# Kernel tuning notes

Measured on AMD Instinct MI355X. Metric: run time of the kernel, lower is better.

The kernel has to match this reference:

```python
import jax, jax.numpy as jnp
import numpy as np
import math

N, E = 50000, 800000
HID, EDIM, H = 128, 32, 8
D = HID // H            # head_dim = 16
FFN = 4 * HID           # ModelConstants.FFN_EXPANSION_FACTOR = 4
EPS = 1e-5


def layer_norm(x, g, b):
    mu = jnp.mean(x, axis=-1, keepdims=True)
    var = jnp.var(x, axis=-1, keepdims=True)
    return (x - mu) * jax.lax.rsqrt(var + EPS) * g + b


def setup_inputs() -> dict:
    key = jax.random.key(0)
    ks = jax.random.split(key, 16)
    s = 1.0 / math.sqrt(HID)
    inp = {
        "x": jax.random.normal(ks[0], (N, HID), jnp.float32),
        "edge_index": jax.random.randint(ks[1], (2, E), 0, N, jnp.int32),
        "edge_attr": jax.random.normal(ks[2], (E, EDIM), jnp.float32),
        # projections stored as (in, out): y = x @ W + b (same math as torch Linear)
        "qW": jax.random.normal(ks[3], (HID, HID), jnp.float32) * s,
        "qb": jnp.zeros((HID,), jnp.float32),
        "kW": jax.random.normal(ks[4], (HID, HID), jnp.float32) * s,
        "kb": jnp.zeros((HID,), jnp.float32),
        "vW": jax.random.normal(ks[5], (HID, HID), jnp.float32) * s,
        "vb": jnp.zeros((HID,), jnp.float32),
        "eW": jax.random.normal(ks[6], (EDIM, H), jnp.float32) / math.sqrt(EDIM),
        "eb": jnp.zeros((H,), jnp.float32),
        "oW": jax.random.normal(ks[7], (HID, HID), jnp.float32) * s,
        "ob": jnp.zeros((HID,), jnp.float32),
        "ln1_g": jnp.ones((HID,), jnp.float32),
        "ln1_b": jnp.zeros((HID,), jnp.float32),
        "f1W": jax.random.normal(ks[8], (HID, FFN), jnp.float32) * s,
        "f1b": jnp.zeros((FFN,), jnp.float32),
        "lnf_g": jnp.ones((FFN,), jnp.float32),
        "lnf_b": jnp.zeros((FFN,), jnp.float32),
        "f2W": jax.random.normal(ks[9], (FFN, HID), jnp.float32) / math.sqrt(FFN),
        "f2b": jnp.zeros((HID,), jnp.float32),
        "ln2_g": jnp.ones((HID,), jnp.float32),
        "ln2_b": jnp.zeros((HID,), jnp.float32),
    }
    return inp


def reference(x, edge_index, edge_attr, qW, qb, kW, kb, vW, vb, eW, eb, oW, ob,
              ln1_g, ln1_b, f1W, f1b, lnf_g, lnf_b, f2W, f2b, ln2_g, ln2_b):
    src, dst = edge_index[0], edge_index[1]
    q = (x @ qW + qb).reshape(N, H, D)
    k = (x @ kW + kb).reshape(N, H, D)
    v = (x @ vW + vb).reshape(N, H, D)
    edge_bias = edge_attr @ eW + eb                     # (E, H)
    # per-edge attention scores
    scores = jnp.sum(q[src] * k[dst], axis=-1) / math.sqrt(D) + edge_bias  # (E, H)
    # scatter softmax over edges grouped by dst
    mx = jax.ops.segment_max(scores, dst, num_segments=N)  # (N, H), -inf for empty
    mx = jnp.where(jnp.isinf(mx), jnp.zeros_like(mx), mx)
    ex = jnp.exp(scores - mx[dst])                      # (E, H)
    den = jax.ops.segment_sum(ex, dst, num_segments=N)
    den = jnp.maximum(den, 1e-8)
    attn = ex / den[dst]                                # (E, H)
    # weighted aggregation
    wv = v[src] * attn[:, :, None]                      # (E, H, D)
    out = jax.ops.segment_sum(wv, dst, num_segments=N)  # (N, H, D)
    out = out.reshape(N, HID) @ oW + ob
    x = layer_norm(x + out, ln1_g, ln1_b)
    h = x @ f1W + f1b
    h = jax.nn.gelu(layer_norm(h, lnf_g, lnf_b), approximate=False)
    h = h @ f2W + f2b
    x = layer_norm(x + h, ln2_g, ln2_b)
    return x
```

## Files before the change

kernel.cpp:

```cpp
#include <hip/hip_runtime.h>
#include <math.h>

#define LN_EPS 1e-5f

typedef __attribute__((ext_vector_type(8))) __bf16 bf16x8;
typedef __attribute__((ext_vector_type(4))) float f32x4;

__device__ inline float bf2f(unsigned short u) {
  union { unsigned int i; float f; } x; x.i = ((unsigned int)u) << 16; return x.f;
}
__device__ inline unsigned short f2bf(float f) {
  union { float f; unsigned int i; } x; x.f = f;
  unsigned int r = (x.i + 0x7FFFu + ((x.i >> 16) & 1u)) >> 16;
  return (unsigned short)r;
}
__device__ inline void gload_lds16(const void* g, void* l) {
  __builtin_amdgcn_global_load_lds((const __attribute__((address_space(1))) void*)g,
                                   (__attribute__((address_space(3))) void*)l, 16, 0, 0);
}

__global__ __launch_bounds__(256)
void to_bf16(const float* __restrict__ in, unsigned short* __restrict__ outp, long n) {
  long i = ((long)blockIdx.x * 256 + threadIdx.x) * 4;
  if (i >= n) return;
  float4 v = *(const float4*)&in[i];
  ushort4 o = { f2bf(v.x), f2bf(v.y), f2bf(v.z), f2bf(v.w) };
  *(ushort4*)&outp[i] = o;
}

struct WDesc { const float* W; unsigned short* Wt; int K, M, ntx; };
__global__ __launch_bounds__(256)
void prep_weights(const float* qW, const float* kW, const float* vW, const float* oW,
                  const float* f1W, const float* f2W,
                  unsigned short* qkvWt, unsigned short* oWt,
                  unsigned short* f1Wt, unsigned short* f2Wt,
                  const float* qb, const float* kb, const float* vb, float* qkvbias) {
  const int t = blockIdx.x;
  if (t == 192) {
    int i = threadIdx.x;
    if (i < 128) { qkvbias[i] = qb[i]; qkvbias[128 + i] = kb[i]; }
    else if (i < 256) qkvbias[256 + (i - 128)] = vb[i - 128];
    return;
  }
  const float* W; unsigned short* Wt; int K, M, lt;
  if (t < 64)       { K = 128; M = 128; lt = t & 15;
    if (t < 16)      { W = qW; Wt = qkvWt; }
    else if (t < 32) { W = kW; Wt = qkvWt + 16384; }
    else if (t < 48) { W = vW; Wt = qkvWt + 32768; }
    else             { W = oW; Wt = oWt; } }
  else if (t < 128) { K = 128; M = 512; lt = t - 64; W = f1W; Wt = f1Wt; }
  else              { K = 512; M = 128; lt = t - 128; W = f2W; Wt = f2Wt; }
  const int ktiles = K >> 5;
  const int k0 = (lt % ktiles) * 32, m0 = (lt / ktiles) * 32;
  __shared__ float tb[32][33];
  const int tx = threadIdx.x & 31, ty = threadIdx.x >> 5;
#pragma unroll
  for (int i = 0; i < 32; i += 8)
    tb[ty + i][tx] = W[(size_t)(k0 + ty + i) * M + m0 + tx];
  __syncthreads();
#pragma unroll
  for (int i = 0; i < 32; i += 8)
    Wt[(size_t)(m0 + ty + i) * K + k0 + tx] = f2bf(tb[tx][ty + i]);
}

template<bool OBF>
__global__ __launch_bounds__(256)
void gemm_mfma(const unsigned short* __restrict__ A, const unsigned short* __restrict__ Wt,
               const float* __restrict__ bias, void* __restrict__ Cout,
               int Nr, int K, int M) {
  __shared__ __align__(16) unsigned short As[128 * 64];
  __shared__ __align__(16) unsigned short Bs[128 * 64];
  const int tid = threadIdx.x;
  const int bm = blockIdx.x * 128, bn = blockIdx.y * 128;
  const int lane = tid & 63;
  const int wr = (tid >> 6) >> 1, wc = (tid >> 6) & 1;
  f32x4 acc[4][4] = {};
  const int nkt = K >> 6;
  for (int kt = 0; kt < nkt; ++kt) {
#pragma unroll
    for (int i = 0; i < 4; ++i) {
      int c = tid + i * 256;
      int row = c >> 3;
      int j = (c & 7) ^ (row & 7);
      int ar = bm + row; ar = ar < Nr ? ar : Nr - 1;
      gload_lds16(A + (size_t)ar * K + kt * 64 + j * 8, As + (size_t)c * 8);
      gload_lds16(Wt + (size_t)(bn + row) * K + kt * 64 + j * 8, Bs + (size_t)c * 8);
    }
    __syncthreads();
#pragma unroll
    for (int ks = 0; ks < 2; ++ks) {
      bf16x8 af[4], bfr[4];
#pragma unroll
      for (int f = 0; f < 4; ++f) {
        int rowa = wr * 64 + f * 16 + (lane & 15);
        int ja = (ks * 4 + (lane >> 4)) ^ (rowa & 7);
        af[f] = *(const bf16x8*)(As + rowa * 64 + ja * 8);
        int rowb = wc * 64 + f * 16 + (lane & 15);
        int jb = (ks * 4 + (lane >> 4)) ^ (rowb & 7);
        bfr[f] = *(const bf16x8*)(Bs + rowb * 64 + jb * 8);
      }
#pragma unroll
      for (int fr = 0; fr < 4; ++fr)
#pragma unroll
        for (int fc = 0; fc < 4; ++fc)
          acc[fr][fc] = __builtin_amdgcn_mfma_f32_16x16x32_bf16(af[fr], bfr[fc], acc[fr][fc], 0, 0, 0);
    }
    __syncthreads();
  }
#pragma unroll
  for (int fr = 0; fr < 4; ++fr) {
#pragma unroll
    for (int j = 0; j < 4; ++j) {
      int row = bm + wr * 64 + fr * 16 + (lane >> 4) * 4 + j;
      if (row < Nr) {
#pragma unroll
        for (int fc = 0; fc < 4; ++fc) {
          int col = bn + wc * 64 + fc * 16 + (lane & 15);
          float v = acc[fr][fc][j] + bias[col];
          if (OBF) ((unsigned short*)Cout)[(size_t)row * M + col] = f2bf(v);
          else     ((float*)Cout)[(size_t)row * M + col] = v;
        }
      }
    }
  }
}

template<bool WF32, bool WBF, bool RESBF>
__global__ __launch_bounds__(256)
void gemm_ln(const unsigned short* __restrict__ A, const unsigned short* __restrict__ Wt,
             const float* __restrict__ bias, const void* __restrict__ res,
             const float* __restrict__ g, const float* __restrict__ b,
             float* __restrict__ y, unsigned short* __restrict__ ybf, int Nr, int K) {
  __shared__ __align__(16) unsigned short As[128 * 64];
  __shared__ __align__(16) unsigned short Bs[128 * 64];
  __shared__ float pls[128][2], plss[128][2];
  const int tid = threadIdx.x;
  const int bm = blockIdx.x * 128;
  const int lane = tid & 63;
  const int wr = (tid >> 6) >> 1, wc = (tid >> 6) & 1;
  f32x4 acc[4][4] = {};
  const int nkt = K >> 6;
  for (int kt = 0; kt < nkt; ++kt) {
#pragma unroll
    for (int i = 0; i < 4; ++i) {
      int c = tid + i * 256;
      int row = c >> 3;
      int j = (c & 7) ^ (row & 7);
      int ar = bm + row; ar = ar < Nr ? ar : Nr - 1;
      gload_lds16(A + (size_t)ar * K + kt * 64 + j * 8, As + (size_t)c * 8);
      gload_lds16(Wt + (size_t)row * K + kt * 64 + j * 8, Bs + (size_t)c * 8);
    }
    __syncthreads();
#pragma unroll
    for (int ks = 0; ks < 2; ++ks) {
      bf16x8 af[4], bfr[4];
#pragma unroll
      for (int f = 0; f < 4; ++f) {
        int rowa = wr * 64 + f * 16 + (lane & 15);
        int ja = (ks * 4 + (lane >> 4)) ^ (rowa & 7);
        af[f] = *(const bf16x8*)(As + rowa * 64 + ja * 8);
        int rowb = wc * 64 + f * 16 + (lane & 15);
        int jb = (ks * 4 + (lane >> 4)) ^ (rowb & 7);
        bfr[f] = *(const bf16x8*)(Bs + rowb * 64 + jb * 8);
      }
#pragma unroll
      for (int fr = 0; fr < 4; ++fr)
#pragma unroll
        for (int fc = 0; fc < 4; ++fc)
          acc[fr][fc] = __builtin_amdgcn_mfma_f32_16x16x32_bf16(af[fr], bfr[fc], acc[fr][fc], 0, 0, 0);
    }
    __syncthreads();
  }
#pragma unroll
  for (int fr = 0; fr < 4; ++fr) {
#pragma unroll
    for (int j = 0; j < 4; ++j) {
      const int rl = wr * 64 + fr * 16 + (lane >> 4) * 4 + j;
      const int row = bm + rl;
      const int rowc = row < Nr ? row : Nr - 1;
      float s = 0.f, ss = 0.f;
#pragma unroll
      for (int fc = 0; fc < 4; ++fc) {
        int col = wc * 64 + fc * 16 + (lane & 15);
        float rv = RESBF ? bf2f(((const unsigned short*)res)[(size_t)rowc * 128 + col])
                         : ((const float*)res)[(size_t)rowc * 128 + col];
        float val = acc[fr][fc][j] + bias[col] + rv;
        acc[fr][fc][j] = val;
        s += val; ss += val * val;
      }
      s += __shfl_xor(s, 1); ss += __shfl_xor(ss, 1);
      s += __shfl_xor(s, 2); ss += __shfl_xor(ss, 2);
      s += __shfl_xor(s, 4); ss += __shfl_xor(ss, 4);
      s += __shfl_xor(s, 8); ss += __shfl_xor(ss, 8);
      if ((lane & 15) == 0) { pls[rl][wc] = s; plss[rl][wc] = ss; }
    }
  }
  __syncthreads();
#pragma unroll
  for (int fr = 0; fr < 4; ++fr) {
#pragma unroll
    for (int j = 0; j < 4; ++j) {
      const int rl = wr * 64 + fr * 16 + (lane >> 4) * 4 + j;
      const int row = bm + rl;
      if (row >= Nr) continue;
      const float S = pls[rl][0] + pls[rl][1];
      const float SS = plss[rl][0] + plss[rl][1];
      const float mu = S * (1.f / 128.f);
      const float inv = rsqrtf(SS * (1.f / 128.f) - mu * mu + LN_EPS);
#pragma unroll
      for (int fc = 0; fc < 4; ++fc) {
        int col = wc * 64 + fc * 16 + (lane & 15);
        float o = (acc[fr][fc][j] - mu) * inv * g[col] + b[col];
        if (WF32) y[(size_t)row * 128 + col] = o;
        if (WBF)  ybf[(size_t)row * 128 + col] = f2bf(o);
      }
    }
  }
}

__global__ __launch_bounds__(256)
void edge_hist(const int* __restrict__ ei, int* __restrict__ deg, int E) {
  int e = blockIdx.x * 256 + threadIdx.x;
  if (e < E) atomicAdd(&deg[ei[E + e]], 1);
}

__global__ __launch_bounds__(256)
void deg_block_sum(const int* __restrict__ deg, int* __restrict__ bsum, int N) {
  const int t = threadIdx.x;
  const int beg = blockIdx.x * 2048 + t * 8;
  int s = 0;
#pragma unroll
  for (int j = 0; j < 8; ++j) { int i = beg + j; if (i < N) s += deg[i]; }
#pragma unroll
  for (int off = 32; off; off >>= 1) s += __shfl_xor(s, off);
  __shared__ int ws[4];
  if ((t & 63) == 0) ws[t >> 6] = s;
  __syncthreads();
  if (t == 0) bsum[blockIdx.x] = ws[0] + ws[1] + ws[2] + ws[3];
}

__global__ __launch_bounds__(64)
void scan_bsum(int* __restrict__ bsum, int* __restrict__ offs_last, int nb) {
  const int t = threadIdx.x;
  int v = (t < nb) ? bsum[t] : 0;
  int inc = v;
#pragma unroll
  for (int off = 1; off < 64; off <<= 1) {
    int x = __shfl_up(inc, off);
    if (t >= off) inc += x;
  }
  if (t < nb) bsum[t] = inc - v;
  if (t == 63) *offs_last = inc;
}

__global__ __launch_bounds__(256)
void deg_scan_write(const int* __restrict__ deg, const int* __restrict__ bsum,
                    int* __restrict__ offs, int* __restrict__ pos, int N) {
  const int t = threadIdx.x;
  const int beg = blockIdx.x * 2048 + t * 8;
  int loc[8]; int T = 0;
#pragma unroll
  for (int j = 0; j < 8; ++j) { int i = beg + j; loc[j] = (i < N) ? deg[i] : 0; T += loc[j]; }
  int inc = T;
#pragma unroll
  for (int off = 1; off < 64; off <<= 1) {
    int x = __shfl_up(inc, off);
    if ((t & 63) >= off) inc += x;
  }
  __shared__ int ws[4];
  if ((t & 63) == 63) ws[t >> 6] = inc;
  __syncthreads();
  const int wid = t >> 6;
  int wbase = 0;
  for (int w = 0; w < wid; ++w) wbase += ws[w];
  int base = bsum[blockIdx.x] + wbase + inc - T;
#pragma unroll
  for (int j = 0; j < 8; ++j) {
    int i = beg + j;
    if (i < N) { offs[i] = base; pos[i] = base; base += loc[j]; }
  }
}

__global__ __launch_bounds__(256)
void edge_scatter_bias(const int* __restrict__ ei, int* __restrict__ pos,
                       const float* __restrict__ ea, const float* __restrict__ eW,
                       const float* __restrict__ eb, int* __restrict__ csr_src,
                       unsigned short* __restrict__ ebp, int E) {
  __shared__ float ews[256];
  __shared__ float ebs[8];
  const int tid = threadIdx.x;
  if (tid < 256) ews[tid] = eW[tid];
  if (tid < 8) ebs[tid] = eb[tid];
  __syncthreads();
  int e = blockIdx.x * 256 + tid;
  if (e >= E) return;
  float bias[8];
#pragma unroll
  for (int h = 0; h < 8; ++h) bias[h] = ebs[h];
#pragma unroll
  for (int i4 = 0; i4 < 8; ++i4) {
    float4 a = *(const float4*)&ea[(size_t)e * 32 + i4 * 4];
    float av[4] = {a.x, a.y, a.z, a.w};
#pragma unroll
    for (int j = 0; j < 4; ++j)
#pragma unroll
      for (int h = 0; h < 8; ++h) bias[h] += av[j] * ews[(i4 * 4 + j) * 8 + h];
  }
  int d = ei[E + e];
  int p = atomicAdd(&pos[d], 1);
  csr_src[p] = ei[e];
  union { unsigned short us[8]; uint4 v; } pk;
#pragma unroll
  for (int h = 0; h < 8; ++h) pk.us[h] = f2bf(bias[h]);
  *(uint4*)&ebp[(size_t)p * 8] = pk.v;
}

__global__ __launch_bounds__(256)
void node_agg(const int* __restrict__ csr_src, const int* __restrict__ offs,
              const unsigned short* __restrict__ qkv, const unsigned short* __restrict__ ebp,
              unsigned short* __restrict__ agg, int N) {
  const int wid = threadIdx.x >> 6, lane = threadIdx.x & 63;
  const int h = lane >> 3;
  const long n = (long)blockIdx.x * 4 + wid;
  if (n >= N) return;
  const int off = offs[n], end = offs[n + 1];
  const ushort2 kv2 = *(const ushort2*)&qkv[(size_t)n * 384 + 128 + lane * 2];
  const float k0 = bf2f(kv2.x), k1 = bf2f(kv2.y);
  float acc0 = 0.f, acc1 = 0.f, den = 0.f;
  int i = off;
  for (; i + 8 <= end; i += 8) {
    size_t bb[8];
#pragma unroll
    for (int u = 0; u < 8; ++u) bb[u] = (size_t)csr_src[i + u] * 384;
    ushort2 qv[8], vv[8];
#pragma unroll
    for (int u = 0; u < 8; ++u) qv[u] = *(const ushort2*)&qkv[bb[u] + lane * 2];
#pragma unroll
    for (int u = 0; u < 8; ++u) vv[u] = *(const ushort2*)&qkv[bb[u] + 256 + lane * 2];
    float ebv[8];
#pragma unroll
    for (int u = 0; u < 8; ++u) ebv[u] = bf2f(ebp[(size_t)(i + u) * 8 + h]);
    float p[8];
#pragma unroll
    for (int u = 0; u < 8; ++u) p[u] = bf2f(qv[u].x) * k0 + bf2f(qv[u].y) * k1;
#pragma unroll
    for (int u = 0; u < 8; ++u) {
      p[u] += __shfl_xor(p[u], 1);
      p[u] += __shfl_xor(p[u], 2);
      p[u] += __shfl_xor(p[u], 4);
    }
#pragma unroll
    for (int u = 0; u < 8; ++u) {
      const float ex = __expf(p[u] * 0.25f + ebv[u]);
      den += ex;
      acc0 += bf2f(vv[u].x) * ex;
      acc1 += bf2f(vv[u].y) * ex;
    }
  }
  for (; i + 4 <= end; i += 4) {
    size_t bb[4];
#pragma unroll
    for (int u = 0; u < 4; ++u) bb[u] = (size_t)csr_src[i + u] * 384;
    ushort2 qv[4], vv[4];
#pragma unroll
    for (int u = 0; u < 4; ++u) qv[u] = *(const ushort2*)&qkv[bb[u] + lane * 2];
#pragma unroll
    for (int u = 0; u < 4; ++u) vv[u] = *(const ushort2*)&qkv[bb[u] + 256 + lane * 2];
    float ebv[4];
#pragma unroll
    for (int u = 0; u < 4; ++u) ebv[u] = bf2f(ebp[(size_t)(i + u) * 8 + h]);
    float p[4];
#pragma unroll
    for (int u = 0; u < 4; ++u) p[u] = bf2f(qv[u].x) * k0 + bf2f(qv[u].y) * k1;
#pragma unroll
    for (int u = 0; u < 4; ++u) {
      p[u] += __shfl_xor(p[u], 1);
      p[u] += __shfl_xor(p[u], 2);
      p[u] += __shfl_xor(p[u], 4);
    }
#pragma unroll
    for (int u = 0; u < 4; ++u) {
      const float ex = __expf(p[u] * 0.25f + ebv[u]);
      den += ex;
      acc0 += bf2f(vv[u].x) * ex;
      acc1 += bf2f(vv[u].y) * ex;
    }
  }
  for (; i < end; ++i) {
    const size_t b0 = (size_t)csr_src[i] * 384;
    const ushort2 qa = *(const ushort2*)&qkv[b0 + lane * 2];
    const ushort2 va = *(const ushort2*)&qkv[b0 + 256 + lane * 2];
    float p = bf2f(qa.x) * k0 + bf2f(qa.y) * k1;
    p += __shfl_xor(p, 1);
    p += __shfl_xor(p, 2);
    p += __shfl_xor(p, 4);
    const float ex = __expf(p * 0.25f + bf2f(ebp[(size_t)i * 8 + h]));
    den += ex;
    acc0 += bf2f(va.x) * ex;
    acc1 += bf2f(va.y) * ex;
  }
  const float r = 1.f / fmaxf(den, 1e-8f);
  ushort2 o; o.x = f2bf(acc0 * r); o.y = f2bf(acc1 * r);
  *(ushort2*)&agg[(size_t)n * 128 + lane * 2] = o;
}

__global__ __launch_bounds__(256)
void ln_gelu512(unsigned short* __restrict__ hbuf, const float* __restrict__ g,
                const float* __restrict__ b, int Nr) {
  __shared__ float rs[4], rss[4];
  const long row = blockIdx.x;
  const int tid = threadIdx.x;
  ushort2 u = *(ushort2*)&hbuf[row * 512 + tid * 2];
  float v0 = bf2f(u.x), v1 = bf2f(u.y);
  float s = v0 + v1, ss = v0 * v0 + v1 * v1;
#pragma unroll
  for (int off = 32; off; off >>= 1) { s += __shfl_xor(s, off); ss += __shfl_xor(ss, off); }
  const int wid = tid >> 6, lane = tid & 63;
  if (lane == 0) { rs[wid] = s; rss[wid] = ss; }
  __syncthreads();
  s = rs[0] + rs[1] + rs[2] + rs[3];
  ss = rss[0] + rss[1] + rss[2] + rss[3];
  const float mu = s * (1.f / 512.f);
  const float inv = rsqrtf(ss * (1.f / 512.f) - mu * mu + LN_EPS);
  float t0 = (v0 - mu) * inv * g[tid * 2] + b[tid * 2];
  float t1 = (v1 - mu) * inv * g[tid * 2 + 1] + b[tid * 2 + 1];
  t0 = 0.5f * t0 * (1.f + erff(t0 * 0.70710678118654752f));
  t1 = 0.5f * t1 * (1.f + erff(t1 * 0.70710678118654752f));
  ushort2 o; o.x = f2bf(t0); o.y = f2bf(t1);
  *(ushort2*)&hbuf[row * 512 + tid * 2] = o;
}

extern "C" void kernel_launch(void* const* d_in, const int* in_sizes, int n_in,
                              void* d_out, int out_size, void* d_ws, size_t ws_size,
                              hipStream_t stream) {
  const float* x   = (const float*)d_in[0];
  const int*   ei  = (const int*)d_in[1];
  const float* ea  = (const float*)d_in[2];
  const float* qW  = (const float*)d_in[3];
  const float* qbi = (const float*)d_in[4];
  const float* kW  = (const float*)d_in[5];
  const float* kbi = (const float*)d_in[6];
  const float* vW  = (const float*)d_in[7];
  const float* vbi = (const float*)d_in[8];
  const float* eW  = (const float*)d_in[9];
  const float* eb  = (const float*)d_in[10];
  const float* oW  = (const float*)d_in[11];
  const float* ob  = (const float*)d_in[12];
  const float* ln1_g = (const float*)d_in[13];
  const float* ln1_b = (const float*)d_in[14];
  const float* f1W = (const float*)d_in[15];
  const float* f1b = (const float*)d_in[16];
  const float* lnf_g = (const float*)d_in[17];
  const float* lnf_b = (const float*)d_in[18];
  const float* f2W = (const float*)d_in[19];
  const float* f2b = (const float*)d_in[20];
  const float* ln2_g = (const float*)d_in[21];
  const float* ln2_b = (const float*)d_in[22];
  float* out = (float*)d_out;

  const int N = in_sizes[0] / 128;
  const int E = in_sizes[1] / 2;
  const size_t NH = (size_t)N * 128;

  float* F = (float*)d_ws;
  unsigned short* xbf   = (unsigned short*)F;
  unsigned short* qkvb  = (unsigned short*)(F + NH / 2);
  unsigned short* ebp   = (unsigned short*)(F + 2 * NH);
  unsigned short* aggb  = (unsigned short*)(F + 2 * NH + NH / 2);
  unsigned short* x1bf  = xbf;
  unsigned short* hbufb = (unsigned short*)(F + NH / 2);
  int* ib      = (int*)(F + 4 * NH);
  int* csr_src = ib;
  int* offs    = ib + E;
  int* pos     = ib + E + N + 1;
  int* bsum    = ib + E + 2 * N + 1;
  unsigned short* wt = (unsigned short*)(ib + E + 2 * N + 128);
  unsigned short* qkvWt = wt;
  unsigned short* oWt   = wt + 49152;
  unsigned short* f1Wt  = wt + 65536;
  unsigned short* f2Wt  = wt + 131072;
  float* qkvbias = (float*)(wt + 196608);

  dim3 blk(256);
  dim3 gqkv((N + 127) / 128, 3);
  dim3 g128((N + 127) / 128, 1);
  dim3 gf1((N + 127) / 128, 4);
  const int nb = (N + 2047) / 2048;
  const int ge = (E + 255) / 256;

  to_bf16<<<dim3((int)((NH / 4 + 255) / 256)), blk, 0, stream>>>(x, xbf, (long)NH);
  prep_weights<<<dim3(193), blk, 0, stream>>>(qW, kW, vW, oW, f1W, f2W,
                                              qkvWt, oWt, f1Wt, f2Wt,
                                              qbi, kbi, vbi, qkvbias);

  gemm_mfma<true><<<gqkv, blk, 0, stream>>>(xbf, qkvWt, qkvbias, qkvb, N, 128, 384);

  hipMemsetAsync(pos, 0, (size_t)N * sizeof(int), stream);
  edge_hist<<<dim3(ge), blk, 0, stream>>>(ei, pos, E);
  deg_block_sum<<<dim3(nb), blk, 0, stream>>>(pos, bsum, N);
  scan_bsum<<<dim3(1), dim3(64), 0, stream>>>(bsum, offs + N, nb);
  deg_scan_write<<<dim3(nb), blk, 0, stream>>>(pos, bsum, offs, pos, N);
  edge_scatter_bias<<<dim3(ge), blk, 0, stream>>>(ei, pos, ea, eW, eb, csr_src, ebp, E);

  node_agg<<<dim3((N + 3) / 4), blk, 0, stream>>>(csr_src, offs, qkvb, ebp, aggb, N);

  gemm_ln<false, true, false><<<g128, blk, 0, stream>>>(aggb, oWt, ob, x,
                                                        ln1_g, ln1_b, nullptr, x1bf, N, 128);

  gemm_mfma<true><<<gf1, blk, 0, stream>>>(x1bf, f1Wt, f1b, hbufb, N, 128, 512);
  ln_gelu512<<<dim3(N), blk, 0, stream>>>(hbufb, lnf_g, lnf_b, N);
  gemm_ln<true, false, true><<<g128, blk, 0, stream>>>(hbufb, f2Wt, f2b, x1bf,
                                                       ln2_g, ln2_b, out, nullptr, N, 512);
}
```

Before: 315.6 us.

## Fuse FFN1 GEMM with LayerNorm+GELU and split edge bias from scatter

Replaces the separate FFN1 GEMM and per-row LN+GELU kernel with a single kernel. Each block computes all 512 output columns for 128 rows, accumulates the row statistics, and then rereads its own rows to apply LayerNorm and GELU. Edge-bias computation moves into the histogram pass, writing a sequential bias buffer, so the scatter kernel only permutes 16-byte records. The LN1 GEMM now reads the bf16 copy of x as its residual instead of fp32. The costs are lower grid parallelism in the fused FFN kernel, an extra E×8 bf16 intermediate buffer, and a residual rounded to bf16.

```diff
diff --git a/kernel.cpp b/kernel.cpp
--- a/kernel.cpp
+++ b/kernel.cpp
@@ -28,7 +28,6 @@
   *(ushort4*)&outp[i] = o;
 }
 
-struct WDesc { const float* W; unsigned short* Wt; int K, M, ntx; };
 __global__ __launch_bounds__(256)
 void prep_weights(const float* qW, const float* kW, const float* vW, const float* oW,
                   const float* f1W, const float* f2W,
@@ -219,73 +218,105 @@
 }
 
 __global__ __launch_bounds__(256)
-void edge_hist(const int* __restrict__ ei, int* __restrict__ deg, int E) {
-  int e = blockIdx.x * 256 + threadIdx.x;
-  if (e < E) atomicAdd(&deg[ei[E + e]], 1);
-}
-
-__global__ __launch_bounds__(256)
-void deg_block_sum(const int* __restrict__ deg, int* __restrict__ bsum, int N) {
-  const int t = threadIdx.x;
-  const int beg = blockIdx.x * 2048 + t * 8;
-  int s = 0;
-#pragma unroll
-  for (int j = 0; j < 8; ++j) { int i = beg + j; if (i < N) s += deg[i]; }
-#pragma unroll
-  for (int off = 32; off; off >>= 1) s += __shfl_xor(s, off);
-  __shared__ int ws[4];
-  if ((t & 63) == 0) ws[t >> 6] = s;
-  __syncthreads();
-  if (t == 0) bsum[blockIdx.x] = ws[0] + ws[1] + ws[2] + ws[3];
-}
-
-__global__ __launch_bounds__(64)
-void scan_bsum(int* __restrict__ bsum, int* __restrict__ offs_last, int nb) {
-  const int t = threadIdx.x;
-  int v = (t < nb) ? bsum[t] : 0;
-  int inc = v;
-#pragma unroll
-  for (int off = 1; off < 64; off <<= 1) {
-    int x = __shfl_up(inc, off);
-    if (t >= off) inc += x;
-  }
-  if (t < nb) bsum[t] = inc - v;
-  if (t == 63) *offs_last = inc;
-}
-
-__global__ __launch_bounds__(256)
-void deg_scan_write(const int* __restrict__ deg, const int* __restrict__ bsum,
-                    int* __restrict__ offs, int* __restrict__ pos, int N) {
-  const int t = threadIdx.x;
-  const int beg = blockIdx.x * 2048 + t * 8;
-  int loc[8]; int T = 0;
-#pragma unroll
-  for (int j = 0; j < 8; ++j) { int i = beg + j; loc[j] = (i < N) ? deg[i] : 0; T += loc[j]; }
-  int inc = T;
-#pragma unroll
-  for (int off = 1; off < 64; off <<= 1) {
-    int x = __shfl_up(inc, off);
-    if ((t & 63) >= off) inc += x;
-  }
-  __shared__ int ws[4];
-  if ((t & 63) == 63) ws[t >> 6] = inc;
-  __syncthreads();
-  const int wid = t >> 6;
-  int wbase = 0;
-  for (int w = 0; w < wid; ++w) wbase += ws[w];
-  int base = bsum[blockIdx.x] + wbase + inc - T;
-#pragma unroll
-  for (int j = 0; j < 8; ++j) {
-    int i = beg + j;
-    if (i < N) { offs[i] = base; pos[i] = base; base += loc[j]; }
-  }
-}
-
-__global__ __launch_bounds__(256)
-void edge_scatter_bias(const int* __restrict__ ei, int* __restrict__ pos,
-                       const float* __restrict__ ea, const float* __restrict__ eW,
-                       const float* __restrict__ eb, int* __restrict__ csr_src,
-                       unsigned short* __restrict__ ebp, int E) {
+void gemm_f1_lngelu(const unsigned short* __restrict__ A, const unsigned short* __restrict__ Wt,
+                    const float* __restrict__ bias, const float* __restrict__ g,
+                    const float* __restrict__ b, unsigned short* __restrict__ hbuf, int Nr) {
+  __shared__ __align__(16) unsigned short As[128 * 64];
+  __shared__ __align__(16) unsigned short Bs[128 * 64];
+  __shared__ float pls[128][2], plss[128][2];
+  __shared__ float rsum[128], rssum[128];
+  __shared__ float glds[512], blds[512];
+  const int tid = threadIdx.x;
+  const int bm = blockIdx.x * 128;
+  const int lane = tid & 63;
+  const int wr = (tid >> 6) >> 1, wc = (tid >> 6) & 1;
+  if (tid < 128) { rsum[tid] = 0.f; rssum[tid] = 0.f; }
+#pragma unroll
+  for (int i = 0; i < 2; ++i) { glds[tid + i * 256] = g[tid + i * 256]; blds[tid + i * 256] = b[tid + i * 256]; }
+  for (int ns = 0; ns < 4; ++ns) {
+    f32x4 acc[4][4] = {};
+#pragma unroll
+    for (int kt = 0; kt < 2; ++kt) {
+#pragma unroll
+      for (int i = 0; i < 4; ++i) {
+        int c = tid + i * 256;
+        int row = c >> 3;
+        int j = (c & 7) ^ (row & 7);
+        int ar = bm + row; ar = ar < Nr ? ar : Nr - 1;
+        gload_lds16(A + (size_t)ar * 128 + kt * 64 + j * 8, As + (size_t)c * 8);
+        gload_lds16(Wt + (size_t)(ns * 128 + row) * 128 + kt * 64 + j * 8, Bs + (size_t)c * 8);
+      }
+      __syncthreads();
+#pragma unroll
+      for (int ks = 0; ks < 2; ++ks) {
+        bf16x8 af[4], bfr[4];
+#pragma unroll
+        for (int f = 0; f < 4; ++f) {
+          int rowa = wr * 64 + f * 16 + (lane & 15);
+          int ja = (ks * 4 + (lane >> 4)) ^ (rowa & 7);
+          af[f] = *(const bf16x8*)(As + rowa * 64 + ja * 8);
+          int rowb = wc * 64 + f * 16 + (lane & 15);
+          int jb = (ks * 4 + (lane >> 4)) ^ (rowb & 7);
+          bfr[f] = *(const bf16x8*)(Bs + rowb * 64 + jb * 8);
+        }
+#pragma unroll
+        for (int fr = 0; fr < 4; ++fr)
+#pragma unroll
+          for (int fc = 0; fc < 4; ++fc)
+            acc[fr][fc] = __builtin_amdgcn_mfma_f32_16x16x32_bf16(af[fr], bfr[fc], acc[fr][fc], 0, 0, 0);
+      }
+      __syncthreads();
+    }
+#pragma unroll
+    for (int fr = 0; fr < 4; ++fr) {
+#pragma unroll
+      for (int j = 0; j < 4; ++j) {
+        const int rl = wr * 64 + fr * 16 + (lane >> 4) * 4 + j;
+        const int row = bm + rl;
+        float s = 0.f, ss = 0.f;
+#pragma unroll
+        for (int fc = 0; fc < 4; ++fc) {
+          int cl = wc * 64 + fc * 16 + (lane & 15);
+          int col = ns * 128 + cl;
+          float val = acc[fr][fc][j] + bias[col];
+          if (row < Nr) hbuf[(size_t)row * 512 + col] = f2bf(val);
+          s += val; ss += val * val;
+        }
+        s += __shfl_xor(s, 1); ss += __shfl_xor(ss, 1);
+        s += __shfl_xor(s, 2); ss += __shfl_xor(ss, 2);
+        s += __shfl_xor(s, 4); ss += __shfl_xor(ss, 4);
+        s += __shfl_xor(s, 8); ss += __shfl_xor(ss, 8);
+        if ((lane & 15) == 0) { pls[rl][wc] = s; plss[rl][wc] = ss; }
+      }
+    }
+    __syncthreads();
+    if (tid < 128) { rsum[tid] += pls[tid][0] + pls[tid][1]; rssum[tid] += plss[tid][0] + plss[tid][1]; }
+    __syncthreads();
+  }
+  for (int it = 0; it < 32; ++it) {
+    int idx = tid + it * 256;
+    int row = idx >> 6, ch = idx & 63;
+    int grow = bm + row;
+    if (grow >= Nr) continue;
+    const float mu = rsum[row] * (1.f / 512.f);
+    const float inv = rsqrtf(rssum[row] * (1.f / 512.f) - mu * mu + LN_EPS);
+    union { uint4 v; unsigned short us[8]; } pk;
+    pk.v = *(const uint4*)&hbuf[(size_t)grow * 512 + ch * 8];
+#pragma unroll
+    for (int j = 0; j < 8; ++j) {
+      int col = ch * 8 + j;
+      float t0 = (bf2f(pk.us[j]) - mu) * inv * glds[col] + blds[col];
+      t0 = 0.5f * t0 * (1.f + erff(t0 * 0.70710678118654752f));
+      pk.us[j] = f2bf(t0);
+    }
+    *(uint4*)&hbuf[(size_t)grow * 512 + ch * 8] = pk.v;
+  }
+}
+
+__global__ __launch_bounds__(256)
+void edge_hist_bias(const int* __restrict__ ei, const float* __restrict__ ea,
+                    const float* __restrict__ eW, const float* __restrict__ eb,
+                    int* __restrict__ deg, unsigned short* __restrict__ ebias_seq, int E) {
   __shared__ float ews[256];
   __shared__ float ebs[8];
   const int tid = threadIdx.x;
@@ -294,6 +325,7 @@
   __syncthreads();
   int e = blockIdx.x * 256 + tid;
   if (e >= E) return;
+  atomicAdd(&deg[ei[E + e]], 1);
   float bias[8];
 #pragma unroll
   for (int h = 0; h < 8; ++h) bias[h] = ebs[h];
@@ -306,13 +338,80 @@
 #pragma unroll
       for (int h = 0; h < 8; ++h) bias[h] += av[j] * ews[(i4 * 4 + j) * 8 + h];
   }
+  union { unsigned short us[8]; uint4 v; } pk;
+#pragma unroll
+  for (int h = 0; h < 8; ++h) pk.us[h] = f2bf(bias[h]);
+  *(uint4*)&ebias_seq[(size_t)e * 8] = pk.v;
+}
+
+__global__ __launch_bounds__(256)
+void deg_block_sum(const int* __restrict__ deg, int* __restrict__ bsum, int N) {
+  const int t = threadIdx.x;
+  const int beg = blockIdx.x * 2048 + t * 8;
+  int s = 0;
+#pragma unroll
+  for (int j = 0; j < 8; ++j) { int i = beg + j; if (i < N) s += deg[i]; }
+#pragma unroll
+  for (int off = 32; off; off >>= 1) s += __shfl_xor(s, off);
+  __shared__ int ws[4];
+  if ((t & 63) == 0) ws[t >> 6] = s;
+  __syncthreads();
+  if (t == 0) bsum[blockIdx.x] = ws[0] + ws[1] + ws[2] + ws[3];
+}
+
+__global__ __launch_bounds__(64)
+void scan_bsum(int* __restrict__ bsum, int* __restrict__ offs_last, int nb) {
+  const int t = threadIdx.x;
+  int v = (t < nb) ? bsum[t] : 0;
+  int inc = v;
+#pragma unroll
+  for (int off = 1; off < 64; off <<= 1) {
+    int x = __shfl_up(inc, off);
+    if (t >= off) inc += x;
+  }
+  if (t < nb) bsum[t] = inc - v;
+  if (t == 63) *offs_last = inc;
+}
+
+__global__ __launch_bounds__(256)
+void deg_scan_write(const int* __restrict__ deg, const int* __restrict__ bsum,
+                    int* __restrict__ offs, int* __restrict__ pos, int N) {
+  const int t = threadIdx.x;
+  const int beg = blockIdx.x * 2048 + t * 8;
+  int loc[8]; int T = 0;
+#pragma unroll
+  for (int j = 0; j < 8; ++j) { int i = beg + j; loc[j] = (i < N) ? deg[i] : 0; T += loc[j]; }
+  int inc = T;
+#pragma unroll
+  for (int off = 1; off < 64; off <<= 1) {
+    int x = __shfl_up(inc, off);
+    if ((t & 63) >= off) inc += x;
+  }
+  __shared__ int ws[4];
+  if ((t & 63) == 63) ws[t >> 6] = inc;
+  __syncthreads();
+  const int wid = t >> 6;
+  int wbase = 0;
+  for (int w = 0; w < wid; ++w) wbase += ws[w];
+  int base = bsum[blockIdx.x] + wbase + inc - T;
+#pragma unroll
+  for (int j = 0; j < 8; ++j) {
+    int i = beg + j;
+    if (i < N) { offs[i] = base; pos[i] = base; base += loc[j]; }
+  }
+}
+
+__global__ __launch_bounds__(256)
+void edge_scatter_pb(const int* __restrict__ ei, int* __restrict__ pos,
+                     const unsigned short* __restrict__ ebias_seq,
+                     int* __restrict__ csr_src, unsigned short* __restrict__ ebp, int E) {
+  int e = blockIdx.x * 256 + threadIdx.x;
+  if (e >= E) return;
   int d = ei[E + e];
+  uint4 pk = *(const uint4*)&ebias_seq[(size_t)e * 8];
   int p = atomicAdd(&pos[d], 1);
   csr_src[p] = ei[e];
-  union { unsigned short us[8]; uint4 v; } pk;
-#pragma unroll
-  for (int h = 0; h < 8; ++h) pk.us[h] = f2bf(bias[h]);
-  *(uint4*)&ebp[(size_t)p * 8] = pk.v;
+  *(uint4*)&ebp[(size_t)p * 8] = pk;
 }
 
 __global__ __launch_bounds__(256)
@@ -402,32 +501,6 @@
   const float r = 1.f / fmaxf(den, 1e-8f);
   ushort2 o; o.x = f2bf(acc0 * r); o.y = f2bf(acc1 * r);
   *(ushort2*)&agg[(size_t)n * 128 + lane * 2] = o;
-}
-
-__global__ __launch_bounds__(256)
-void ln_gelu512(unsigned short* __restrict__ hbuf, const float* __restrict__ g,
-                const float* __restrict__ b, int Nr) {
-  __shared__ float rs[4], rss[4];
-  const long row = blockIdx.x;
-  const int tid = threadIdx.x;
-  ushort2 u = *(ushort2*)&hbuf[row * 512 + tid * 2];
-  float v0 = bf2f(u.x), v1 = bf2f(u.y);
-  float s = v0 + v1, ss = v0 * v0 + v1 * v1;
-#pragma unroll
-  for (int off = 32; off; off >>= 1) { s += __shfl_xor(s, off); ss += __shfl_xor(ss, off); }
-  const int wid = tid >> 6, lane = tid & 63;
-  if (lane == 0) { rs[wid] = s; rss[wid] = ss; }
-  __syncthreads();
-  s = rs[0] + rs[1] + rs[2] + rs[3];
-  ss = rss[0] + rss[1] + rss[2] + rss[3];
-  const float mu = s * (1.f / 512.f);
-  const float inv = rsqrtf(ss * (1.f / 512.f) - mu * mu + LN_EPS);
-  float t0 = (v0 - mu) * inv * g[tid * 2] + b[tid * 2];
-  float t1 = (v1 - mu) * inv * g[tid * 2 + 1] + b[tid * 2 + 1];
-  t0 = 0.5f * t0 * (1.f + erff(t0 * 0.70710678118654752f));
-  t1 = 0.5f * t1 * (1.f + erff(t1 * 0.70710678118654752f));
-  ushort2 o; o.x = f2bf(t0); o.y = f2bf(t1);
-  *(ushort2*)&hbuf[row * 512 + tid * 2] = o;
 }
 
 extern "C" void kernel_launch(void* const* d_in, const int* in_sizes, int n_in,
@@ -467,6 +540,7 @@
   unsigned short* qkvb  = (unsigned short*)(F + NH / 2);
   unsigned short* ebp   = (unsigned short*)(F + 2 * NH);
   unsigned short* aggb  = (unsigned short*)(F + 2 * NH + NH / 2);
+  unsigned short* ebias_seq = (unsigned short*)(F + 3 * NH);
   unsigned short* x1bf  = xbf;
   unsigned short* hbufb = (unsigned short*)(F + NH / 2);
   int* ib      = (int*)(F + 4 * NH);
@@ -484,7 +558,6 @@
   dim3 blk(256);
   dim3 gqkv((N + 127) / 128, 3);
   dim3 g128((N + 127) / 128, 1);
-  dim3 gf1((N + 127) / 128, 4);
   const int nb = (N + 2047) / 2048;
   const int ge = (E + 255) / 256;
 
@@ -496,19 +569,18 @@
   gemm_mfma<true><<<gqkv, blk, 0, stream>>>(xbf, qkvWt, qkvbias, qkvb, N, 128, 384);
 
   hipMemsetAsync(pos, 0, (size_t)N * sizeof(int), stream);
-  edge_hist<<<dim3(ge), blk, 0, stream>>>(ei, pos, E);
+  edge_hist_bias<<<dim3(ge), blk, 0, stream>>>(ei, ea, eW, eb, pos, ebias_seq, E);
   deg_block_sum<<<dim3(nb), blk, 0, stream>>>(pos, bsum, N);
   scan_bsum<<<dim3(1), dim3(64), 0, stream>>>(bsum, offs + N, nb);
   deg_scan_write<<<dim3(nb), blk, 0, stream>>>(pos, bsum, offs, pos, N);
-  edge_scatter_bias<<<dim3(ge), blk, 0, stream>>>(ei, pos, ea, eW, eb, csr_src, ebp, E);
+  edge_scatter_pb<<<dim3(ge), blk, 0, stream>>>(ei, pos, ebias_seq, csr_src, ebp, E);
 
   node_agg<<<dim3((N + 3) / 4), blk, 0, stream>>>(csr_src, offs, qkvb, ebp, aggb, N);
 
-  gemm_ln<false, true, false><<<g128, blk, 0, stream>>>(aggb, oWt, ob, x,
-                                                        ln1_g, ln1_b, nullptr, x1bf, N, 128);
-
-  gemm_mfma<true><<<gf1, blk, 0, stream>>>(x1bf, f1Wt, f1b, hbufb, N, 128, 512);
-  ln_gelu512<<<dim3(N), blk, 0, stream>>>(hbufb, lnf_g, lnf_b, N);
+  gemm_ln<false, true, true><<<g128, blk, 0, stream>>>(aggb, oWt, ob, xbf,
+                                                       ln1_g, ln1_b, nullptr, x1bf, N, 128);
+
+  gemm_f1_lngelu<<<g128, blk, 0, stream>>>(x1bf, f1Wt, f1b, lnf_g, lnf_b, hbufb, N);
   gemm_ln<true, false, true><<<g128, blk, 0, stream>>>(hbufb, f2Wt, f2b, x1bf,
                                                        ln2_g, ln2_b, out, nullptr, N, 512);
 }
```

After: 317.1 us. Within noise of the previous version (+0.5%).

## Fuse FFN LayerNorm+GELU into GEMMs and merge prologue kernels

Applied to the files above, without the earlier changes.

Removes the separate ln_gelu512 pass over the 512-wide hidden buffer. The f1 GEMM now emits per-row partial sum and sum-of-squares, and the f2 GEMM applies normalization and erf-GELU to its A fragments in registers before the MFMAs. The bf16 conversion, the pos zeroing and the weight prep are merged into one launch. The LN1 residual now reads bf16 x instead of fp32. In exchange the GELU is recomputed redundantly in both column-waves inside the GEMM inner loop, and the residual path loses precision.

```diff
diff --git a/kernel.cpp b/kernel.cpp
--- a/kernel.cpp
+++ b/kernel.cpp
@@ -20,24 +20,32 @@
 }
 
 __global__ __launch_bounds__(256)
-void to_bf16(const float* __restrict__ in, unsigned short* __restrict__ outp, long n) {
-  long i = ((long)blockIdx.x * 256 + threadIdx.x) * 4;
-  if (i >= n) return;
-  float4 v = *(const float4*)&in[i];
-  ushort4 o = { f2bf(v.x), f2bf(v.y), f2bf(v.z), f2bf(v.w) };
-  *(ushort4*)&outp[i] = o;
-}
-
-struct WDesc { const float* W; unsigned short* Wt; int K, M, ntx; };
-__global__ __launch_bounds__(256)
-void prep_weights(const float* qW, const float* kW, const float* vW, const float* oW,
-                  const float* f1W, const float* f2W,
-                  unsigned short* qkvWt, unsigned short* oWt,
-                  unsigned short* f1Wt, unsigned short* f2Wt,
-                  const float* qb, const float* kb, const float* vb, float* qkvbias) {
-  const int t = blockIdx.x;
+void front(const float* __restrict__ x, unsigned short* __restrict__ xbf, long n,
+           int* __restrict__ pos, int N, int gA, int gZ,
+           const float* qW, const float* kW, const float* vW, const float* oW,
+           const float* f1W, const float* f2W,
+           unsigned short* qkvWt, unsigned short* oWt,
+           unsigned short* f1Wt, unsigned short* f2Wt,
+           const float* qb, const float* kb, const float* vb, float* qkvbias) {
+  const int b = blockIdx.x;
+  const int tid = threadIdx.x;
+  if (b < gA) {
+    long i = ((long)b * 256 + tid) * 4;
+    if (i >= n) return;
+    float4 v = *(const float4*)&x[i];
+    ushort4 o = { f2bf(v.x), f2bf(v.y), f2bf(v.z), f2bf(v.w) };
+    *(ushort4*)&xbf[i] = o;
+    return;
+  }
+  if (b < gA + gZ) {
+    int base = (b - gA) * 1024 + tid * 4;
+    if (base + 3 < N) *(int4*)(pos + base) = make_int4(0, 0, 0, 0);
+    else for (int j = 0; j < 4; ++j) if (base + j < N) pos[base + j] = 0;
+    return;
+  }
+  const int t = b - gA - gZ;
   if (t == 192) {
-    int i = threadIdx.x;
+    int i = tid;
     if (i < 128) { qkvbias[i] = qb[i]; qkvbias[128 + i] = kb[i]; }
     else if (i < 256) qkvbias[256 + (i - 128)] = vb[i - 128];
     return;
@@ -53,7 +61,7 @@
   const int ktiles = K >> 5;
   const int k0 = (lt % ktiles) * 32, m0 = (lt / ktiles) * 32;
   __shared__ float tb[32][33];
-  const int tx = threadIdx.x & 31, ty = threadIdx.x >> 5;
+  const int tx = tid & 31, ty = tid >> 5;
 #pragma unroll
   for (int i = 0; i < 32; i += 8)
     tb[ty + i][tx] = W[(size_t)(k0 + ty + i) * M + m0 + tx];
@@ -63,13 +71,14 @@
     Wt[(size_t)(m0 + ty + i) * K + k0 + tx] = f2bf(tb[tx][ty + i]);
 }
 
-template<bool OBF>
+template<bool OBF, bool STATS>
 __global__ __launch_bounds__(256)
 void gemm_mfma(const unsigned short* __restrict__ A, const unsigned short* __restrict__ Wt,
                const float* __restrict__ bias, void* __restrict__ Cout,
-               int Nr, int K, int M) {
+               float2* __restrict__ rpart, int Np, int Nr, int K, int M) {
   __shared__ __align__(16) unsigned short As[128 * 64];
   __shared__ __align__(16) unsigned short Bs[128 * 64];
+  __shared__ float spls[128][2], splss[128][2];
   const int tid = threadIdx.x;
   const int bm = blockIdx.x * 128, bn = blockIdx.y * 128;
   const int lane = tid & 63;
@@ -111,33 +120,72 @@
   for (int fr = 0; fr < 4; ++fr) {
 #pragma unroll
     for (int j = 0; j < 4; ++j) {
-      int row = bm + wr * 64 + fr * 16 + (lane >> 4) * 4 + j;
-      if (row < Nr) {
-#pragma unroll
-        for (int fc = 0; fc < 4; ++fc) {
-          int col = bn + wc * 64 + fc * 16 + (lane & 15);
-          float v = acc[fr][fc][j] + bias[col];
+      const int rl = wr * 64 + fr * 16 + (lane >> 4) * 4 + j;
+      const int row = bm + rl;
+      float s = 0.f, ss = 0.f;
+#pragma unroll
+      for (int fc = 0; fc < 4; ++fc) {
+        int col = bn + wc * 64 + fc * 16 + (lane & 15);
+        float v = acc[fr][fc][j] + bias[col];
+        if (row < Nr) {
           if (OBF) ((unsigned short*)Cout)[(size_t)row * M + col] = f2bf(v);
           else     ((float*)Cout)[(size_t)row * M + col] = v;
         }
-      }
-    }
-  }
-}
-
-template<bool WF32, bool WBF, bool RESBF>
+        s += v; ss += v * v;
+      }
+      if (STATS) {
+        s += __shfl_xor(s, 1); ss += __shfl_xor(ss, 1);
+        s += __shfl_xor(s, 2); ss += __shfl_xor(ss, 2);
+        s += __shfl_xor(s, 4); ss += __shfl_xor(ss, 4);
+        s += __shfl_xor(s, 8); ss += __shfl_xor(ss, 8);
+        if ((lane & 15) == 0) { spls[rl][wc] = s; splss[rl][wc] = ss; }
+      }
+    }
+  }
+  if (STATS) {
+    __syncthreads();
+    if (tid < 128) {
+      int row = bm + tid;
+      if (row < Nr)
+        rpart[(size_t)blockIdx.y * Np + row] =
+            make_float2(spls[tid][0] + spls[tid][1], splss[tid][0] + splss[tid][1]);
+    }
+  }
+}
+
+template<bool WF32, bool WBF, bool RESBF, bool ALN>
 __global__ __launch_bounds__(256)
 void gemm_ln(const unsigned short* __restrict__ A, const unsigned short* __restrict__ Wt,
              const float* __restrict__ bias, const void* __restrict__ res,
              const float* __restrict__ g, const float* __restrict__ b,
-             float* __restrict__ y, unsigned short* __restrict__ ybf, int Nr, int K) {
+             float* __restrict__ y, unsigned short* __restrict__ ybf,
+             const float2* __restrict__ rpart, int Np,
+             const float* __restrict__ ag, const float* __restrict__ ab,
+             int Nr, int K) {
   __shared__ __align__(16) unsigned short As[128 * 64];
   __shared__ __align__(16) unsigned short Bs[128 * 64];
   __shared__ float pls[128][2], plss[128][2];
+  __shared__ float muv[128], invv[128];
+  __shared__ float aglds[512], ablds[512];
   const int tid = threadIdx.x;
   const int bm = blockIdx.x * 128;
   const int lane = tid & 63;
   const int wr = (tid >> 6) >> 1, wc = (tid >> 6) & 1;
+  if (ALN) {
+    if (tid < 128) {
+      int row = bm + tid; row = row < Nr ? row : Nr - 1;
+      float2 p0 = rpart[row], p1 = rpart[(size_t)Np + row];
+      float2 p2 = rpart[2 * (size_t)Np + row], p3 = rpart[3 * (size_t)Np + row];
+      float s = (p0.x + p1.x) + (p2.x + p3.x);
+      float ss = (p0.y + p1.y) + (p2.y + p3.y);
+      float mu = s * (1.f / 512.f);
+      muv[tid] = mu;
+      invv[tid] = rsqrtf(ss * (1.f / 512.f) - mu * mu + LN_EPS);
+    }
+    aglds[tid] = ag[tid]; aglds[256 + tid] = ag[256 + tid];
+    ablds[tid] = ab[tid]; ablds[256 + tid] = ab[256 + tid];
+    __syncthreads();
+  }
   f32x4 acc[4][4] = {};
   const int nkt = K >> 6;
   for (int kt = 0; kt < nkt; ++kt) {
@@ -162,6 +210,23 @@
         int rowb = wc * 64 + f * 16 + (lane & 15);
         int jb = (ks * 4 + (lane >> 4)) ^ (rowb & 7);
         bfr[f] = *(const bf16x8*)(Bs + rowb * 64 + jb * 8);
+      }
+      if (ALN) {
+        const int colbase = kt * 64 + (ks * 4 + (lane >> 4)) * 8;
+#pragma unroll
+        for (int f = 0; f < 4; ++f) {
+          const int rowa = wr * 64 + f * 16 + (lane & 15);
+          const float mu = muv[rowa], inv = invv[rowa];
+          union { bf16x8 v; unsigned short us[8]; } ua;
+          ua.v = af[f];
+#pragma unroll
+          for (int el = 0; el < 8; ++el) {
+            float t = (bf2f(ua.us[el]) - mu) * inv * aglds[colbase + el] + ablds[colbase + el];
+            t = 0.5f * t * (1.f + erff(t * 0.70710678118654752f));
+            ua.us[el] = f2bf(t);
+          }
+          af[f] = ua.v;
+        }
       }
 #pragma unroll
       for (int fr = 0; fr < 4; ++fr)
@@ -402,32 +467,6 @@
   const float r = 1.f / fmaxf(den, 1e-8f);
   ushort2 o; o.x = f2bf(acc0 * r); o.y = f2bf(acc1 * r);
   *(ushort2*)&agg[(size_t)n * 128 + lane * 2] = o;
-}
-
-__global__ __launch_bounds__(256)
-void ln_gelu512(unsigned short* __restrict__ hbuf, const float* __restrict__ g,
-                const float* __restrict__ b, int Nr) {
-  __shared__ float rs[4], rss[4];
-  const long row = blockIdx.x;
-  const int tid = threadIdx.x;
-  ushort2 u = *(ushort2*)&hbuf[row * 512 + tid * 2];
-  float v0 = bf2f(u.x), v1 = bf2f(u.y);
-  float s = v0 + v1, ss = v0 * v0 + v1 * v1;
-#pragma unroll
-  for (int off = 32; off; off >>= 1) { s += __shfl_xor(s, off); ss += __shfl_xor(ss, off); }
-  const int wid = tid >> 6, lane = tid & 63;
-  if (lane == 0) { rs[wid] = s; rss[wid] = ss; }
-  __syncthreads();
-  s = rs[0] + rs[1] + rs[2] + rs[3];
-  ss = rss[0] + rss[1] + rss[2] + rss[3];
-  const float mu = s * (1.f / 512.f);
-  const float inv = rsqrtf(ss * (1.f / 512.f) - mu * mu + LN_EPS);
-  float t0 = (v0 - mu) * inv * g[tid * 2] + b[tid * 2];
-  float t1 = (v1 - mu) * inv * g[tid * 2 + 1] + b[tid * 2 + 1];
-  t0 = 0.5f * t0 * (1.f + erff(t0 * 0.70710678118654752f));
-  t1 = 0.5f * t1 * (1.f + erff(t1 * 0.70710678118654752f));
-  ushort2 o; o.x = f2bf(t0); o.y = f2bf(t1);
-  *(ushort2*)&hbuf[row * 512 + tid * 2] = o;
 }
 
 extern "C" void kernel_launch(void* const* d_in, const int* in_sizes, int n_in,
@@ -469,6 +508,7 @@
   unsigned short* aggb  = (unsigned short*)(F + 2 * NH + NH / 2);
   unsigned short* x1bf  = xbf;
   unsigned short* hbufb = (unsigned short*)(F + NH / 2);
+  float2* rpart = (float2*)(F + 3 * NH);
   int* ib      = (int*)(F + 4 * NH);
   int* csr_src = ib;
   int* offs    = ib + E;
@@ -487,15 +527,17 @@
   dim3 gf1((N + 127) / 128, 4);
   const int nb = (N + 2047) / 2048;
   const int ge = (E + 255) / 256;
-
-  to_bf16<<<dim3((int)((NH / 4 + 255) / 256)), blk, 0, stream>>>(x, xbf, (long)NH);
-  prep_weights<<<dim3(193), blk, 0, stream>>>(qW, kW, vW, oW, f1W, f2W,
-                                              qkvWt, oWt, f1Wt, f2Wt,
-                                              qbi, kbi, vbi, qkvbias);
-
-  gemm_mfma<true><<<gqkv, blk, 0, stream>>>(xbf, qkvWt, qkvbias, qkvb, N, 128, 384);
-
-  hipMemsetAsync(pos, 0, (size_t)N * sizeof(int), stream);
+  const int gA = (int)((NH / 4 + 255) / 256);
+  const int gZ = (N + 1023) / 1024;
+
+  front<<<dim3(gA + gZ + 193), blk, 0, stream>>>(x, xbf, (long)NH, pos, N, gA, gZ,
+                                                 qW, kW, vW, oW, f1W, f2W,
+                                                 qkvWt, oWt, f1Wt, f2Wt,
+                                                 qbi, kbi, vbi, qkvbias);
+
+  gemm_mfma<true, false><<<gqkv, blk, 0, stream>>>(xbf, qkvWt, qkvbias, qkvb,
+                                                   nullptr, 0, N, 128, 384);
+
   edge_hist<<<dim3(ge), blk, 0, stream>>>(ei, pos, E);
   deg_block_sum<<<dim3(nb), blk, 0, stream>>>(pos, bsum, N);
   scan_bsum<<<dim3(1), dim3(64), 0, stream>>>(bsum, offs + N, nb);
@@ -504,11 +546,13 @@
 
   node_agg<<<dim3((N + 3) / 4), blk, 0, stream>>>(csr_src, offs, qkvb, ebp, aggb, N);
 
-  gemm_ln<false, true, false><<<g128, blk, 0, stream>>>(aggb, oWt, ob, x,
-                                                        ln1_g, ln1_b, nullptr, x1bf, N, 128);
-
-  gemm_mfma<true><<<gf1, blk, 0, stream>>>(x1bf, f1Wt, f1b, hbufb, N, 128, 512);
-  ln_gelu512<<<dim3(N), blk, 0, stream>>>(hbufb, lnf_g, lnf_b, N);
-  gemm_ln<true, false, true><<<g128, blk, 0, stream>>>(hbufb, f2Wt, f2b, x1bf,
-                                                       ln2_g, ln2_b, out, nullptr, N, 512);
-}
+  gemm_ln<false, true, true, false><<<g128, blk, 0, stream>>>(
+      aggb, oWt, ob, xbf, ln1_g, ln1_b, nullptr, x1bf,
+      nullptr, 0, nullptr, nullptr, N, 128);
+
+  gemm_mfma<true, true><<<gf1, blk, 0, stream>>>(x1bf, f1Wt, f1b, hbufb,
+                                                 (float2*)rpart, N, N, 128, 512);
+  gemm_ln<true, false, true, true><<<g128, blk, 0, stream>>>(
+      hbufb, f2Wt, f2b, x1bf, ln2_g, ln2_b, out, nullptr,
+      (const float2*)rpart, N, lnf_g, lnf_b, N, 512);
+}
```

Result: slower. 393.8 us (+24.8%).
